# Performance work log

Hardware: AMD Instinct MI355X
Metric: run time of the kernel (lower is better)

The kernel has to match this reference:

```python
import jax, jax.numpy as jnp
import numpy as np

N_ENT = 50000
N_REL = 16
D_E = 64
D_R = 64
D_OUT = 32
N_EDGE = 1000000


def setup_inputs() -> dict:
    key = jax.random.key(0)
    ks = jax.random.split(key, 8)
    # 0.1 scale keeps tanh / softmax in a realistic (non-saturated) range,
    # mimicking trained embedding magnitudes.
    entity_table = jax.random.normal(ks[0], (N_ENT, D_E), dtype=jnp.float32) * 0.1
    relation_table = jax.random.normal(ks[1], (N_REL, D_R), dtype=jnp.float32) * 0.1
    W_R = jax.random.normal(ks[2], (N_REL, D_E, D_R), dtype=jnp.float32) * (1.0 / np.sqrt(D_E))
    W1 = jax.random.normal(ks[3], (D_E, D_OUT), dtype=jnp.float32) * (1.0 / np.sqrt(D_E))
    b1 = jnp.zeros((D_OUT,), dtype=jnp.float32)
    W2 = jax.random.normal(ks[4], (D_E, D_OUT), dtype=jnp.float32) * (1.0 / np.sqrt(D_E))
    b2 = jnp.zeros((D_OUT,), dtype=jnp.float32)
    src = jax.random.randint(ks[5], (N_EDGE,), 0, N_ENT, dtype=jnp.int32)
    dst = jax.random.randint(ks[6], (N_EDGE,), 0, N_ENT, dtype=jnp.int32)
    etype = jax.random.randint(ks[7], (N_EDGE,), 0, N_REL, dtype=jnp.int32)
    return {"entity_table": entity_table, "relation_table": relation_table,
            "W_R": W_R, "W1": W1, "b1": b1, "W2": W2, "b2": b2,
            "src": src, "dst": dst, "etype": etype}


def reference(entity_table, relation_table, W_R, W1, b1, W2, b2, src, dst, etype):
    """KGAT calc_att (per-relation edge attention + edge softmax) followed by
    one bi-interaction Aggregator layer (dropout = identity, eval mode)."""
    n_nodes = entity_table.shape[0]
    # Per-relation projection of all node embeddings (grouped GEMM form of the
    # per-relation loop in compute_attention): [R, N, d_r]
    proj = jnp.einsum('nd,rde->rne', entity_table, W_R)
    r_mul_h = proj[etype, src]            # [E, d_r]  h W_r per edge
    r_mul_t = proj[etype, dst]            # [E, d_r]  t W_r per edge
    r_e = relation_table[etype]           # [E, d_r]
    # att = (h W_r) . tanh(t W_r + r)
    att = jnp.sum(r_mul_h * jnp.tanh(r_mul_t + r_e), axis=-1)  # [E]
    # edge softmax grouped by destination node
    att_max = jax.ops.segment_max(att, dst, num_segments=n_nodes)     # [N]
    ex = jnp.exp(att - att_max[dst])
    denom = jax.ops.segment_sum(ex, dst, num_segments=n_nodes)        # [N]
    a = ex / denom[dst]                                               # [E]
    # u_mul_e + sum: N_h[v] = sum_{(u->v)} a_e * node[u]
    msg = a[:, None] * entity_table[src]                              # [E, d]
    N_h = jax.ops.segment_sum(msg, dst, num_segments=n_nodes)         # [N, d]
    node = entity_table
    # bi-interaction aggregator (LeakyReLU slope 0.01, torch default)
    out1 = jax.nn.leaky_relu((node + N_h) @ W1 + b1)
    out2 = jax.nn.leaky_relu((node * N_h) @ W2 + b2)
    return out1 + out2
```

## Files before the change

### kernel.cpp

```cpp
#include <hip/hip_runtime.h>
#include <math.h>

#define NREL 16
#define DE 64
#define DOUT 32

typedef __attribute__((ext_vector_type(8))) short bf16x8;
typedef __attribute__((ext_vector_type(16))) float f32x16;

__device__ __forceinline__ short f2bf(float f) {
    unsigned u = __builtin_bit_cast(unsigned, f);
    unsigned r = (u + 0x7FFFu + ((u >> 16) & 1u)) >> 16;
    return (short)r;
}
__device__ __forceinline__ float bf2f(short s) {
    unsigned u = ((unsigned)(unsigned short)s) << 16;
    return __builtin_bit_cast(float, u);
}
__device__ __forceinline__ unsigned cvt_pk_bf16(float lo, float hi) {
    unsigned r;
    asm("v_cvt_pk_bf16_f32 %0, %1, %2" : "=v"(r) : "v"(lo), "v"(hi));
    return r;
}
__device__ __forceinline__ float tanh_fast(float x) {
    float e = __expf(2.0f * x);
    return fmaf(-2.0f, __builtin_amdgcn_rcpf(e + 1.0f), 1.0f);
}

__global__ __launch_bounds__(256) void hist_kernel(const int* __restrict__ dst,
                                                   int* __restrict__ counts, int E) {
    int i = blockIdx.x * blockDim.x + threadIdx.x;
    if (i < E) atomicAdd(&counts[dst[i]], 1);
}

__global__ __launch_bounds__(256) void blocksum_kernel(const int* __restrict__ counts,
                                                       int* __restrict__ blockSums, int n) {
    __shared__ int wsum[4];
    int i = blockIdx.x * 256 + threadIdx.x;
    int v = (i < n) ? counts[i] : 0;
#pragma unroll
    for (int off = 1; off < 64; off <<= 1) v += __shfl_xor(v, off);
    if ((threadIdx.x & 63) == 0) wsum[threadIdx.x >> 6] = v;
    __syncthreads();
    if (threadIdx.x == 0)
        blockSums[blockIdx.x] = wsum[0] + wsum[1] + wsum[2] + wsum[3];
}

__global__ __launch_bounds__(1024) void blockscan_kernel(int* __restrict__ blockSums, int nb) {
    __shared__ int lds[1024];
    int t = threadIdx.x;
    int v = (t < nb) ? blockSums[t] : 0;
    lds[t] = v;
    __syncthreads();
    for (int off = 1; off < 1024; off <<= 1) {
        int u = (t >= off) ? lds[t - off] : 0;
        __syncthreads();
        lds[t] += u;
        __syncthreads();
    }
    if (t < nb) blockSums[t] = (t == 0) ? 0 : lds[t - 1];
}

__global__ __launch_bounds__(256) void scanout_kernel(const int* __restrict__ counts,
                                                      const int* __restrict__ blockSums,
                                                      int* __restrict__ offsets,
                                                      int* __restrict__ cursor, int n) {
    __shared__ int wsum[4];
    int t = threadIdx.x;
    int i = blockIdx.x * 256 + t;
    int lane = t & 63;
    int w = t >> 6;
    int v = (i < n) ? counts[i] : 0;
    int incl = v;
#pragma unroll
    for (int off = 1; off < 64; off <<= 1) {
        int u = __shfl_up(incl, off);
        if (lane >= off) incl += u;
    }
    if (lane == 63) wsum[w] = incl;
    __syncthreads();
    int woff = 0;
#pragma unroll
    for (int j = 0; j < 4; ++j) if (j < w) woff += wsum[j];
    int excl = incl - v + woff + blockSums[blockIdx.x];
    if (i < n) { offsets[i] = excl; cursor[i] = excl; }
    if (i == n - 1) offsets[n] = excl + v;
}

__global__ __launch_bounds__(256) void scatter_kernel(const int* __restrict__ dst,
                                                      const int* __restrict__ src,
                                                      const int* __restrict__ etype,
                                                      int* __restrict__ cursor,
                                                      int* __restrict__ pks, int E) {
    int i = blockIdx.x * blockDim.x + threadIdx.x;
    if (i < E) {
        int pos = atomicAdd(&cursor[dst[i]], 1);
        pks[pos] = (src[i] << 4) | etype[i];
    }
}

__global__ __launch_bounds__(256) void entcvt_kernel(const float* __restrict__ ent,
                                                     short* __restrict__ entbf, int tot) {
    int i = blockIdx.x * 256 + threadIdx.x;
    if (i < tot) entbf[i] = f2bf(ent[i]);
}

__global__ __launch_bounds__(256) void wcvt_kernel(const float* __restrict__ WR,
                                                   short* __restrict__ Wbf,
                                                   short* __restrict__ WTbf) {
    int i = blockIdx.x * 256 + threadIdx.x;
    int r = i >> 12, k = (i >> 6) & 63, j = i & 63;
    short b = f2bf(WR[i]);
    Wbf[i] = b;
    WTbf[(r << 12) + (j << 6) + k] = b;
}

#define TQ 392
__global__ __launch_bounds__(256) void projq_kernel(const short* __restrict__ entbf,
                                                    const float* __restrict__ rel,
                                                    const short* __restrict__ Wbf,
                                                    const short* __restrict__ WTbf,
                                                    short* __restrict__ Qbf, int N) {
    __shared__ short Tl[4 * 2048];
    int lane = threadIdx.x & 63;
    int wid = threadIdx.x >> 6;
    int lin = blockIdx.x;
    int r = lin / TQ;
    int tq = lin - r * TQ;
    int m0 = (tq * 4 + wid) * 32;
    if (m0 >= N) return;
    int hi = lane >> 5;
    int lo = lane & 31;

    int arow = m0 + lo;
    if (arow >= N) arow = N - 1;
    const short* ap = entbf + ((size_t)arow << 6) + hi * 8;
    bf16x8 A[4];
#pragma unroll
    for (int kk = 0; kk < 4; ++kk) A[kk] = *(const bf16x8*)(ap + kk * 16);

    short* tb = Tl + wid * 2048;
    const short* wtb = WTbf + ((size_t)r << 12);
    const short* wb  = Wbf  + ((size_t)r << 12);

    f32x16 acc0 = {}, acc1 = {};
#pragma unroll
    for (int kk = 0; kk < 4; ++kk) {
        bf16x8 b0 = *(const bf16x8*)(wtb + lo * DE + kk * 16 + hi * 8);
        bf16x8 b1 = *(const bf16x8*)(wtb + (lo + 32) * DE + kk * 16 + hi * 8);
        acc0 = __builtin_amdgcn_mfma_f32_32x32x16_bf16(A[kk], b0, acc0, 0, 0, 0);
        acc1 = __builtin_amdgcn_mfma_f32_32x32x16_bf16(A[kk], b1, acc1, 0, 0, 0);
    }
    float rv0 = rel[r * DE + lo];
    float rv1 = rel[r * DE + 32 + lo];
#pragma unroll
    for (int i = 0; i < 16; ++i) {
        int row = (i & 3) + 8 * (i >> 2) + 4 * hi;
        int sw = (row & 7) << 3;
        unsigned u = cvt_pk_bf16(tanh_fast(acc0[i] + rv0), tanh_fast(acc1[i] + rv1));
        tb[(row * DE + lo) ^ sw] = (short)(u & 0xffff);
        tb[(row * DE + 32 + lo) ^ sw] = (short)(u >> 16);
    }
    bf16x8 A2[4];
#pragma unroll
    for (int kk = 0; kk < 4; ++kk)
        A2[kk] = *(const bf16x8*)(tb + ((lo * DE + kk * 16 + hi * 8) ^ ((lo & 7) << 3)));

    f32x16 q0 = {}, q1 = {};
#pragma unroll
    for (int kk = 0; kk < 4; ++kk) {
        bf16x8 b0 = *(const bf16x8*)(wb + lo * DE + kk * 16 + hi * 8);
        bf16x8 b1 = *(const bf16x8*)(wb + (lo + 32) * DE + kk * 16 + hi * 8);
        q0 = __builtin_amdgcn_mfma_f32_32x32x16_bf16(A2[kk], b0, q0, 0, 0, 0);
        q1 = __builtin_amdgcn_mfma_f32_32x32x16_bf16(A2[kk], b1, q1, 0, 0, 0);
    }
#pragma unroll
    for (int i = 0; i < 16; ++i) {
        int row = (i & 3) + 8 * (i >> 2) + 4 * hi;
        unsigned u = cvt_pk_bf16(q0[i], q1[i]);
        tb[row * DE + lo] = (short)(u & 0xffff);
        tb[row * DE + 32 + lo] = (short)(u >> 16);
    }
#pragma unroll
    for (int p = 0; p < 4; ++p) {
        int row = p * 8 + (lane >> 3);
        int node = m0 + row;
        bf16x8 vq = *(const bf16x8*)(tb + row * DE + (lane & 7) * 8);
        if (node < N)
            *(bf16x8*)(Qbf + (((size_t)r * N + node) << 6) + (lane & 7) * 8) = vq;
    }
}

__global__ __launch_bounds__(256) void agg_kernel(const float* __restrict__ ent,
                                                  const short* __restrict__ entbf,
                                                  const short* __restrict__ Qbf,
                                                  const int* __restrict__ offsets,
                                                  const int* __restrict__ pks,
                                                  const float* __restrict__ W1,
                                                  const float* __restrict__ b1,
                                                  const float* __restrict__ W2,
                                                  const float* __restrict__ b2,
                                                  float* __restrict__ out, int n) {
    __shared__ float xl[4][128];
    int lane = threadIdx.x & 63;
    int wid = threadIdx.x >> 6;
    int v = (blockIdx.x << 2) + wid;
    if (v >= n) return;
    int o0 = offsets[v], o1 = offsets[v + 1];
    int g = lane >> 3, gl = lane & 7;
    const short* qbase = Qbf + ((size_t)v << 6) + gl * 8;

    float m = -INFINITY, l = 0.f;
    float acc[8];
#pragma unroll
    for (int j = 0; j < 8; ++j) acc[j] = 0.f;

    int k = o0 + g;
    bool val = k < o1;
    bf16x8 xv = {}, qv = {};
    if (val) {
        int pk = pks[k];
        xv = *(const bf16x8*)(entbf + ((size_t)(pk >> 4) << 6) + gl * 8);
        qv = *(const bf16x8*)(qbase + (((unsigned)(pk & 15) * (unsigned)n) << 6));
    }
    int iters = (o1 - o0 + 7) >> 3;
    for (int it = 0; it < iters; ++it) {
        int kn = k + 8;
        bool valn = kn < o1;
        bf16x8 xn = {}, qn = {};
        if (valn) {
            int pk = pks[kn];
            xn = *(const bf16x8*)(entbf + ((size_t)(pk >> 4) << 6) + gl * 8);
            qn = *(const bf16x8*)(qbase + (((unsigned)(pk & 15) * (unsigned)n) << 6));
        }
        float xf[8];
        float d = 0.f;
#pragma unroll
        for (int j = 0; j < 8; ++j) {
            xf[j] = bf2f(xv[j]);
            d = fmaf(xf[j], bf2f(qv[j]), d);
        }
        d += __shfl_xor(d, 1);
        d += __shfl_xor(d, 2);
        d += __shfl_xor(d, 4);
        float p = val ? d : -INFINITY;
        float nm = fmaxf(m, p);
        float sc, pe;
        if (nm == -INFINITY) { sc = 0.f; pe = 0.f; }
        else { sc = __expf(m - nm); pe = __expf(p - nm); }
        l = l * sc + pe;
#pragma unroll
        for (int j = 0; j < 8; ++j) acc[j] = fmaf(acc[j], sc, pe * xf[j]);
        m = nm;
        k = kn; val = valn; xv = xn; qv = qn;
    }
#pragma unroll
    for (int off = 8; off < 64; off <<= 1) {
        float mo = __shfl_xor(m, off);
        float lo2 = __shfl_xor(l, off);
        float nm = fmaxf(m, mo);
        float s1 = (nm == -INFINITY) ? 0.f : __expf(m - nm);
        float s2 = (nm == -INFINITY) ? 0.f : __expf(mo - nm);
        l = l * s1 + lo2 * s2;
#pragma unroll
        for (int j = 0; j < 8; ++j) {
            float ao = __shfl_xor(acc[j], off);
            acc[j] = acc[j] * s1 + ao * s2;
        }
        m = nm;
    }
    float* xw = &xl[wid][0];
    float invl = (l > 0.f) ? (1.0f / l) : 0.f;
    if (g == 0) {
#pragma unroll
        for (int j = 0; j < 8; ++j) xw[gl * 8 + j] = acc[j] * invl;
    }
    float node = ent[((size_t)v << 6) + lane];
    float Nh = xw[lane];
    float x1 = node + Nh;
    float x2 = node * Nh;
    xw[lane] = x1;
    xw[64 + lane] = x2;
    int j = lane & 31;
    const float* __restrict__ Wsel = (lane < 32) ? W1 : W2;
    float bias = (lane < 32) ? b1[j] : b2[j];
    const float* xb = xw + ((lane < 32) ? 0 : 64);
    float o = 0.f;
#pragma unroll 8
    for (int kk = 0; kk < DE; ++kk)
        o = fmaf(xb[kk], Wsel[kk * DOUT + j], o);
    o += bias;
    float lr = (o > 0.f) ? o : 0.01f * o;
    float other = __shfl_xor(lr, 32);
    if (lane < 32) out[(size_t)v * DOUT + lane] = lr + other;
}

extern "C" void kernel_launch(void* const* d_in, const int* in_sizes, int n_in,
                              void* d_out, int out_size, void* d_ws, size_t ws_size,
                              hipStream_t stream) {
    const float* ent = (const float*)d_in[0];
    const float* rel = (const float*)d_in[1];
    const float* WR  = (const float*)d_in[2];
    const float* W1  = (const float*)d_in[3];
    const float* b1  = (const float*)d_in[4];
    const float* W2  = (const float*)d_in[5];
    const float* b2  = (const float*)d_in[6];
    const int* src   = (const int*)d_in[7];
    const int* dst   = (const int*)d_in[8];
    const int* ety   = (const int*)d_in[9];
    float* out       = (float*)d_out;

    const int E = in_sizes[7];
    const int N = in_sizes[0] / DE;
    const int NB = (N + 255) / 256;

    size_t qElems  = (size_t)N * NREL * DE;
    size_t eElems  = (size_t)N * DE;
    size_t wElems  = (size_t)NREL * DE * DE;

    char* ws = (char*)d_ws;
    short* Qbf   = (short*)ws;
    short* entbf = Qbf + qElems;
    short* Wbf   = entbf + eElems;
    short* WTbf  = Wbf + wElems;
    int* counts  = (int*)(WTbf + wElems);
    int* offsets = counts + N;
    int* cursor  = offsets + N + 1;
    int* pks     = cursor + N;
    int* bsums   = pks + E;
    size_t need  = (size_t)((char*)(bsums + NB) - ws);
    if (ws_size < need) return;

    hipMemsetAsync(counts, 0, (size_t)N * 4, stream);
    entcvt_kernel<<<(int)((eElems + 255) / 256), 256, 0, stream>>>(ent, entbf, (int)eElems);
    wcvt_kernel<<<(int)(wElems / 256), 256, 0, stream>>>(WR, Wbf, WTbf);
    hist_kernel<<<(E + 255) / 256, 256, 0, stream>>>(dst, counts, E);
    blocksum_kernel<<<NB, 256, 0, stream>>>(counts, bsums, N);
    blockscan_kernel<<<1, 1024, 0, stream>>>(bsums, NB);
    scanout_kernel<<<NB, 256, 0, stream>>>(counts, bsums, offsets, cursor, N);
    scatter_kernel<<<(E + 255) / 256, 256, 0, stream>>>(dst, src, ety, cursor, pks, E);
    projq_kernel<<<TQ * NREL, 256, 0, stream>>>(entbf, rel, Wbf, WTbf, Qbf, N);
    agg_kernel<<<(N + 3) / 4, 256, 0, stream>>>(ent, entbf, Qbf, offsets, pks,
                                                W1, b1, W2, b2, out, N);
}
```

Baseline: 249.8 us.

## Partition histogram and scatter atomics by destination range across block groups

The histogram and CSR scatter kernels now launch eight times as many blocks. Each block in a group of eight handles only edges whose destination falls in one of eight node-range partitions. The aim is to localize atomics so that concurrent blocks (likely spread across XCDs by block index) hit disjoint counter ranges, which improves L2 locality and cuts cross-die contention. The cost is that every edge's dst is read eight times and most threads exit idle, which adds launch and memory-read overhead.

```diff
diff --git a/kernel.cpp b/kernel.cpp
--- a/kernel.cpp
+++ b/kernel.cpp
@@ -4,6 +4,7 @@
 #define NREL 16
 #define DE 64
 #define DOUT 32
+#define NPART 8
 
 typedef __attribute__((ext_vector_type(8))) short bf16x8;
 typedef __attribute__((ext_vector_type(16))) float f32x16;
@@ -28,9 +29,15 @@
 }
 
 __global__ __launch_bounds__(256) void hist_kernel(const int* __restrict__ dst,
-                                                   int* __restrict__ counts, int E) {
-    int i = blockIdx.x * blockDim.x + threadIdx.x;
-    if (i < E) atomicAdd(&counts[dst[i]], 1);
+                                                   int* __restrict__ counts,
+                                                   int E, int psz) {
+    int part = blockIdx.x & (NPART - 1);
+    int i = (blockIdx.x >> 3) * 256 + threadIdx.x;
+    if (i < E) {
+        int d = dst[i];
+        if (d >= part * psz && d < (part + 1) * psz)
+            atomicAdd(&counts[d], 1);
+    }
 }
 
 __global__ __launch_bounds__(256) void blocksum_kernel(const int* __restrict__ counts,
@@ -91,11 +98,16 @@
                                                       const int* __restrict__ src,
                                                       const int* __restrict__ etype,
                                                       int* __restrict__ cursor,
-                                                      int* __restrict__ pks, int E) {
-    int i = blockIdx.x * blockDim.x + threadIdx.x;
+                                                      int* __restrict__ pks,
+                                                      int E, int psz) {
+    int part = blockIdx.x & (NPART - 1);
+    int i = (blockIdx.x >> 3) * 256 + threadIdx.x;
     if (i < E) {
-        int pos = atomicAdd(&cursor[dst[i]], 1);
-        pks[pos] = (src[i] << 4) | etype[i];
+        int d = dst[i];
+        if (d >= part * psz && d < (part + 1) * psz) {
+            int pos = atomicAdd(&cursor[d], 1);
+            pks[pos] = (src[i] << 4) | etype[i];
+        }
     }
 }
 
@@ -313,6 +325,8 @@
     const int E = in_sizes[7];
     const int N = in_sizes[0] / DE;
     const int NB = (N + 255) / 256;
+    const int psz = (N + NPART - 1) / NPART;
+    const int chunks = (E + 255) / 256;
 
     size_t qElems  = (size_t)N * NREL * DE;
     size_t eElems  = (size_t)N * DE;
@@ -334,11 +348,11 @@
     hipMemsetAsync(counts, 0, (size_t)N * 4, stream);
     entcvt_kernel<<<(int)((eElems + 255) / 256), 256, 0, stream>>>(ent, entbf, (int)eElems);
     wcvt_kernel<<<(int)(wElems / 256), 256, 0, stream>>>(WR, Wbf, WTbf);
-    hist_kernel<<<(E + 255) / 256, 256, 0, stream>>>(dst, counts, E);
+    hist_kernel<<<chunks * NPART, 256, 0, stream>>>(dst, counts, E, psz);
     blocksum_kernel<<<NB, 256, 0, stream>>>(counts, bsums, N);
     blockscan_kernel<<<1, 1024, 0, stream>>>(bsums, NB);
     scanout_kernel<<<NB, 256, 0, stream>>>(counts, bsums, offsets, cursor, N);
-    scatter_kernel<<<(E + 255) / 256, 256, 0, stream>>>(dst, src, ety, cursor, pks, E);
+    scatter_kernel<<<chunks * NPART, 256, 0, stream>>>(dst, src, ety, cursor, pks, E, psz);
     projq_kernel<<<TQ * NREL, 256, 0, stream>>>(entbf, rel, Wbf, WTbf, Qbf, N);
     agg_kernel<<<(N + 3) / 4, 256, 0, stream>>>(ent, entbf, Qbf, offsets, pks,
                                                 W1, b1, W2, b2, out, N);
```

Measured after the change: 236.2 us. 5.4% less time.
